# Kernel optimization log

Hardware: AMD Instinct MI355X
Metric: run time of the kernel (lower is better)

Reference implementation:

```python
import jax, jax.numpy as jnp
import numpy as np


def setup_inputs() -> dict:
    key = jax.random.key(0)
    ks = jax.random.split(key, 8)
    N, T, U = 8, 512, 64
    E, D, J, V = 512, 512, 512, 500
    s = 0.02
    return {
        "encoder_out": jax.random.normal(ks[0], (N, T, E), jnp.float32),
        "decoder_out": jax.random.normal(ks[1], (N, U, D), jnp.float32),
        "W_enc": jax.random.normal(ks[2], (J, E), jnp.float32) * s,
        "b_enc": jnp.zeros((J,), jnp.float32),
        "W_dec": jax.random.normal(ks[3], (J, D), jnp.float32) * s,
        "b_dec": jnp.zeros((J,), jnp.float32),
        "W_out": jax.random.normal(ks[4], (V, J), jnp.float32) * s,
        "b_out": jnp.zeros((V,), jnp.float32),
    }


def reference(encoder_out, decoder_out, W_enc, b_enc, W_dec, b_dec, W_out, b_out):
    # Project encoder [N,T,E]->[N,T,J] and decoder [N,U,D]->[N,U,J]
    enc = jnp.einsum("nte,je->ntj", encoder_out, W_enc) + b_enc
    dec = jnp.einsum("nud,jd->nuj", decoder_out, W_dec) + b_dec
    # Broadcast add over (T,U), tanh, then vocab projection -> [N,T,U,V]
    activations = jnp.tanh(enc[:, :, None, :] + dec[:, None, :, :])
    logits = jnp.einsum("ntuj,vj->ntuv", activations, W_out) + b_out
    return logits
```

## Files before the change

### kernel.cpp

```cpp
#include <hip/hip_runtime.h>
#include <hip/hip_bf16.h>


typedef __attribute__((ext_vector_type(4))) float f32x4;
typedef __attribute__((ext_vector_type(16))) float f32x16;
typedef __attribute__((ext_vector_type(8))) short s16x8;
typedef __attribute__((ext_vector_type(8))) unsigned short u16x8;

static __device__ __forceinline__ unsigned short f2bf(float x) {
    union { float f; unsigned u; } v; v.f = x;
    return (unsigned short)((v.u + 0x7FFFu + ((v.u >> 16) & 1u)) >> 16);
}

static __device__ __forceinline__ float bf2f(unsigned short u) {
    union { unsigned u; float f; } v; v.u = ((unsigned)u) << 16;
    return v.f;
}

static __device__ __forceinline__ float fast_tanh(float x) {
    float e = __expf(2.0f * x);
    float r = __builtin_amdgcn_rcpf(e + 1.0f);
    return __builtin_fmaf(-2.0f, r, 1.0f);
}

static __device__ __forceinline__ void lbar() {
    asm volatile("s_waitcnt lgkmcnt(0)" ::: "memory");
    __builtin_amdgcn_s_barrier();
    __builtin_amdgcn_sched_barrier(0);
}

static __device__ __forceinline__ unsigned swz64(int r, int c) {
    return (unsigned)(r * 64 + ((c ^ ((r >> 1) & 3)) << 4));
}

static __device__ void proj_body(
    const float* __restrict__ A, const float* __restrict__ W,
    const float* __restrict__ b, unsigned short* __restrict__ C,
    int mt, int jt, unsigned short* As, unsigned short* Bs)
{
    const int tid = threadIdx.x;
    const int lane = tid & 63, wid = tid >> 6;
    const int wm = wid >> 1, wn = wid & 1;

    f32x4 acc[4][4];
    const f32x4 zero = {0.f, 0.f, 0.f, 0.f};
    #pragma unroll
    for (int i = 0; i < 4; ++i)
        #pragma unroll
        for (int j = 0; j < 4; ++j) acc[i][j] = zero;

    const int c8 = (tid & 7) * 8;
    const int rbase = tid >> 3;

    for (int kt = 0; kt < 8; ++kt) {
        __syncthreads();
        #pragma unroll
        for (int p = 0; p < 4; ++p) {
            int r = p * 32 + rbase;
            int byte = (r * 128 + c8 * 2) ^ ((r & 7) << 4);
            {
                const float* s = A + (size_t)(mt * 128 + r) * 512 + kt * 64 + c8;
                f32x4 v0 = *(const f32x4*)s, v1 = *(const f32x4*)(s + 4);
                s16x8 pk;
                pk[0] = (short)f2bf(v0[0]); pk[1] = (short)f2bf(v0[1]);
                pk[2] = (short)f2bf(v0[2]); pk[3] = (short)f2bf(v0[3]);
                pk[4] = (short)f2bf(v1[0]); pk[5] = (short)f2bf(v1[1]);
                pk[6] = (short)f2bf(v1[2]); pk[7] = (short)f2bf(v1[3]);
                *(s16x8*)((char*)As + byte) = pk;
            }
            {
                const float* s = W + (size_t)(jt * 128 + r) * 512 + kt * 64 + c8;
                f32x4 v0 = *(const f32x4*)s, v1 = *(const f32x4*)(s + 4);
                s16x8 pk;
                pk[0] = (short)f2bf(v0[0]); pk[1] = (short)f2bf(v0[1]);
                pk[2] = (short)f2bf(v0[2]); pk[3] = (short)f2bf(v0[3]);
                pk[4] = (short)f2bf(v1[0]); pk[5] = (short)f2bf(v1[1]);
                pk[6] = (short)f2bf(v1[2]); pk[7] = (short)f2bf(v1[3]);
                *(s16x8*)((char*)Bs + byte) = pk;
            }
        }
        __syncthreads();
        #pragma unroll
        for (int kk = 0; kk < 2; ++kk) {
            s16x8 af[4], bfr[4];
            #pragma unroll
            for (int mi = 0; mi < 4; ++mi) {
                int row = wm * 64 + mi * 16 + (lane & 15);
                int byte = (row * 128 + kk * 64 + ((lane >> 4) * 16)) ^ ((row & 7) << 4);
                af[mi] = *(const s16x8*)((const char*)As + byte);
            }
            #pragma unroll
            for (int ni = 0; ni < 4; ++ni) {
                int row = wn * 64 + ni * 16 + (lane & 15);
                int byte = (row * 128 + kk * 64 + ((lane >> 4) * 16)) ^ ((row & 7) << 4);
                bfr[ni] = *(const s16x8*)((const char*)Bs + byte);
            }
            #pragma unroll
            for (int mi = 0; mi < 4; ++mi)
                #pragma unroll
                for (int ni = 0; ni < 4; ++ni)
                    acc[mi][ni] = __builtin_amdgcn_mfma_f32_16x16x32_bf16(
                        af[mi], bfr[ni], acc[mi][ni], 0, 0, 0);
        }
    }

    #pragma unroll
    for (int ni = 0; ni < 4; ++ni) {
        int col = jt * 128 + wn * 64 + ni * 16 + (lane & 15);
        float bias = b[col];
        #pragma unroll
        for (int mi = 0; mi < 4; ++mi) {
            int row0 = mt * 128 + wm * 64 + mi * 16 + ((lane >> 4) << 2);
            #pragma unroll
            for (int j = 0; j < 4; ++j)
                C[(size_t)(row0 + j) * 512 + col] = f2bf(acc[mi][ni][j] + bias);
        }
    }
}

__global__ __launch_bounds__(256) void prep(
    const float* __restrict__ Wout, unsigned short* __restrict__ img,
    const float* __restrict__ encoder_out, const float* __restrict__ W_enc,
    const float* __restrict__ b_enc, unsigned short* __restrict__ enc_p,
    const float* __restrict__ decoder_out, const float* __restrict__ W_dec,
    const float* __restrict__ b_dec, unsigned short* __restrict__ dec_p,
    const float* __restrict__ b_out, float* __restrict__ bpad)
{
    __shared__ unsigned short As[128 * 64];
    __shared__ unsigned short Bs[128 * 64];
    const int b = blockIdx.x;
    if (b < 128) {
        int tid = b * 256 + threadIdx.x;
        int lane = tid & 63;
        int khalf = (tid >> 6) & 1;
        int tile = (tid >> 7) & 15;
        int kt = tid >> 11;
        int v = tile * 32 + (lane & 31);
        int k = kt * 32 + khalf * 16 + (lane >> 5) * 8;
        s16x8 pk = {0, 0, 0, 0, 0, 0, 0, 0};
        if (v < 500) {
            const float* s = Wout + (size_t)v * 512 + k;
            f32x4 a = *(const f32x4*)s, c = *(const f32x4*)(s + 4);
            pk[0] = (short)f2bf(a[0]); pk[1] = (short)f2bf(a[1]);
            pk[2] = (short)f2bf(a[2]); pk[3] = (short)f2bf(a[3]);
            pk[4] = (short)f2bf(c[0]); pk[5] = (short)f2bf(c[1]);
            pk[6] = (short)f2bf(c[2]); pk[7] = (short)f2bf(c[3]);
        }
        *(s16x8*)(img + (size_t)tid * 8) = pk;
    } else if (b < 256) {
        int q = b - 128;
        proj_body(encoder_out, W_enc, b_enc, enc_p, q & 31, q >> 5, As, Bs);
    } else if (b < 272) {
        int q = b - 256;
        proj_body(decoder_out, W_dec, b_dec, dec_p, q & 3, q >> 2, As, Bs);
    } else {
        int i = threadIdx.x;
        bpad[i] = (i < 500) ? b_out[i] : 0.f;
        bpad[i + 256] = (i + 256 < 500) ? b_out[i + 256] : 0.f;
    }
}

__global__ __launch_bounds__(512, 2) void joiner_main(
    const unsigned short* __restrict__ enc, const unsigned short* __restrict__ dec,
    const unsigned short* __restrict__ Wimg, const float* __restrict__ bout,
    float* __restrict__ out)
{
    __shared__ __align__(16) char raw[66048];
    unsigned short* As0 = (unsigned short*)raw;
    unsigned short* As1 = (unsigned short*)(raw + 8192);
    float* ep = (float*)raw;

    const int bid = blockIdx.x;
    const int tid = threadIdx.x, lane = tid & 63, wn = tid >> 6;
    const int n = bid >> 8, tt = bid & 255;

    f32x16 acc[4][2];
    #pragma unroll
    for (int i = 0; i < 4; ++i)
        #pragma unroll
        for (int j = 0; j < 2; ++j)
            #pragma unroll
            for (int e = 0; e < 16; ++e) acc[i][j][e] = 0.f;

    const int r = tid >> 2;
    const int q = tid & 3;
    const int tl = r >> 6, u = r & 63;
    const unsigned short* erow = enc + ((size_t)n * 512 + tt * 2 + tl) * 512 + q * 8;
    const unsigned short* drow = dec + ((size_t)n * 64 + u) * 512 + q * 8;
    const unsigned abyte = swz64(r, q);
    const char* wbase = (const char*)Wimg + (size_t)wn * 4096 + (size_t)lane * 16;
    const int lr = lane & 31, kg = lane >> 5;

    s16x8 bc0, bc1, bc2, bc3;
    u16x8 eN, dN;
    {
        u16x8 e = *(const u16x8*)erow;
        u16x8 d = *(const u16x8*)drow;
        s16x8 p;
        #pragma unroll
        for (int i = 0; i < 8; ++i)
            p[i] = (short)f2bf(fast_tanh(bf2f(e[i]) + bf2f(d[i])));
        *(s16x8*)((char*)As0 + abyte) = p;
        eN = *(const u16x8*)(erow + 32);
        dN = *(const u16x8*)(drow + 32);
        bc0 = *(const s16x8*)(wbase);
        bc1 = *(const s16x8*)(wbase + 1024);
        bc2 = *(const s16x8*)(wbase + 2048);
        bc3 = *(const s16x8*)(wbase + 3072);
    }
    lbar();

    #pragma unroll
    for (int kt = 0; kt < 16; ++kt) {
        const char* Ac = (char*)((kt & 1) ? As1 : As0);
        char* An = (char*)((kt & 1) ? As0 : As1);

        if (kt < 15) {
            s16x8 p;
            #pragma unroll
            for (int i = 0; i < 8; ++i)
                p[i] = (short)f2bf(fast_tanh(bf2f(eN[i]) + bf2f(dN[i])));
            *(s16x8*)(An + abyte) = p;
        }
        if (kt < 14) {
            eN = *(const u16x8*)(erow + (kt + 2) * 32);
            dN = *(const u16x8*)(drow + (kt + 2) * 32);
        }
        s16x8 bn0, bn1, bn2, bn3;
        if (kt < 15) {
            const char* g = wbase + (size_t)(kt + 1) * 32768;
            bn0 = *(const s16x8*)(g);
            bn1 = *(const s16x8*)(g + 1024);
            bn2 = *(const s16x8*)(g + 2048);
            bn3 = *(const s16x8*)(g + 3072);
        }
        {
            s16x8 a0 = *(const s16x8*)(Ac + swz64(lr, kg));
            s16x8 a1 = *(const s16x8*)(Ac + swz64(32 + lr, kg));
            s16x8 a2 = *(const s16x8*)(Ac + swz64(64 + lr, kg));
            s16x8 a3 = *(const s16x8*)(Ac + swz64(96 + lr, kg));
            acc[0][0] = __builtin_amdgcn_mfma_f32_32x32x16_bf16(bc0, a0, acc[0][0], 0, 0, 0);
            acc[0][1] = __builtin_amdgcn_mfma_f32_32x32x16_bf16(bc2, a0, acc[0][1], 0, 0, 0);
            acc[1][0] = __builtin_amdgcn_mfma_f32_32x32x16_bf16(bc0, a1, acc[1][0], 0, 0, 0);
            acc[1][1] = __builtin_amdgcn_mfma_f32_32x32x16_bf16(bc2, a1, acc[1][1], 0, 0, 0);
            acc[2][0] = __builtin_amdgcn_mfma_f32_32x32x16_bf16(bc0, a2, acc[2][0], 0, 0, 0);
            acc[2][1] = __builtin_amdgcn_mfma_f32_32x32x16_bf16(bc2, a2, acc[2][1], 0, 0, 0);
            acc[3][0] = __builtin_amdgcn_mfma_f32_32x32x16_bf16(bc0, a3, acc[3][0], 0, 0, 0);
            acc[3][1] = __builtin_amdgcn_mfma_f32_32x32x16_bf16(bc2, a3, acc[3][1], 0, 0, 0);
        }
        {
            s16x8 a0 = *(const s16x8*)(Ac + swz64(lr, 2 + kg));
            s16x8 a1 = *(const s16x8*)(Ac + swz64(32 + lr, 2 + kg));
            s16x8 a2 = *(const s16x8*)(Ac + swz64(64 + lr, 2 + kg));
            s16x8 a3 = *(const s16x8*)(Ac + swz64(96 + lr, 2 + kg));
            acc[0][0] = __builtin_amdgcn_mfma_f32_32x32x16_bf16(bc1, a0, acc[0][0], 0, 0, 0);
            acc[0][1] = __builtin_amdgcn_mfma_f32_32x32x16_bf16(bc3, a0, acc[0][1], 0, 0, 0);
            acc[1][0] = __builtin_amdgcn_mfma_f32_32x32x16_bf16(bc1, a1, acc[1][0], 0, 0, 0);
            acc[1][1] = __builtin_amdgcn_mfma_f32_32x32x16_bf16(bc3, a1, acc[1][1], 0, 0, 0);
            acc[2][0] = __builtin_amdgcn_mfma_f32_32x32x16_bf16(bc1, a2, acc[2][0], 0, 0, 0);
            acc[2][1] = __builtin_amdgcn_mfma_f32_32x32x16_bf16(bc3, a2, acc[2][1], 0, 0, 0);
            acc[3][0] = __builtin_amdgcn_mfma_f32_32x32x16_bf16(bc1, a3, acc[3][0], 0, 0, 0);
            acc[3][1] = __builtin_amdgcn_mfma_f32_32x32x16_bf16(bc3, a3, acc[3][1], 0, 0, 0);
        }
        lbar();
        bc0 = bn0; bc1 = bn1; bc2 = bn2; bc3 = bn3;
    }

    const int hi4 = kg * 4;
    #pragma unroll
    for (int o = 0; o < 4; ++o) {
        if (o) lbar();
        {
            #pragma unroll
            for (int ni = 0; ni < 2; ++ni) {
                #pragma unroll
                for (int qq = 0; qq < 4; ++qq) {
                    int v4 = wn * 64 + ni * 32 + qq * 8 + hi4;
                    if (v4 < 500) {
                        f32x4 b = *(const f32x4*)(bout + v4);
                        f32x4 ov;
                        ov[0] = acc[o][ni][qq * 4 + 0] + b[0];
                        ov[1] = acc[o][ni][qq * 4 + 1] + b[1];
                        ov[2] = acc[o][ni][qq * 4 + 2] + b[2];
                        ov[3] = acc[o][ni][qq * 4 + 3] + b[3];
                        *(f32x4*)(ep + lr * 516 + v4) = ov;
                    }
                }
            }
        }
        lbar();
        const size_t base =
            (((size_t)n * 512 + tt * 2 + (o >> 1)) * 64 + (o & 1) * 32) * 500;
        #pragma unroll
        for (int i = 0; i < 8; ++i) {
            int idx = i * 512 + tid;
            if (idx < 4000) {
                int rr = idx / 125;
                int vi = (idx - rr * 125) * 4;
                f32x4 ov = *(const f32x4*)(ep + rr * 516 + vi);
                __builtin_nontemporal_store(ov, (f32x4*)(out + base + (size_t)idx * 4));
            }
        }
    }
}

extern "C" void kernel_launch(void* const* d_in, const int* in_sizes, int n_in,
                              void* d_out, int out_size, void* d_ws, size_t ws_size,
                              hipStream_t stream) {
    const float* encoder_out = (const float*)d_in[0];
    const float* decoder_out = (const float*)d_in[1];
    const float* W_enc = (const float*)d_in[2];
    const float* b_enc = (const float*)d_in[3];
    const float* W_dec = (const float*)d_in[4];
    const float* b_dec = (const float*)d_in[5];
    const float* W_out = (const float*)d_in[6];
    const float* b_out = (const float*)d_in[7];
    float* out = (float*)d_out;

    unsigned short* enc_p = (unsigned short*)d_ws;
    unsigned short* dec_p = enc_p + (size_t)4096 * 512;
    unsigned short* wimg  = dec_p + (size_t)512 * 512;
    float* bpad = (float*)(wimg + 262144);

    prep<<<dim3(273), 256, 0, stream>>>(W_out, wimg,
                                        encoder_out, W_enc, b_enc, enc_p,
                                        decoder_out, W_dec, b_dec, dec_p,
                                        b_out, bpad);
    joiner_main<<<dim3(2048), 512, 0, stream>>>(enc_p, dec_p, wimg, bpad, out);
}
```

Measured before the change: 213.9 us.

## Stagger tanh and MFMA order across waves and use packed bf16 conversion

```diff
diff --git a/kernel.cpp b/kernel.cpp
--- a/kernel.cpp
+++ b/kernel.cpp
@@ -5,6 +5,7 @@
 typedef __attribute__((ext_vector_type(4))) float f32x4;
 typedef __attribute__((ext_vector_type(16))) float f32x16;
 typedef __attribute__((ext_vector_type(8))) short s16x8;
+typedef __attribute__((ext_vector_type(4))) unsigned int u32x4;
 typedef __attribute__((ext_vector_type(8))) unsigned short u16x8;
 
 static __device__ __forceinline__ unsigned short f2bf(float x) {
@@ -23,10 +24,16 @@
     return __builtin_fmaf(-2.0f, r, 1.0f);
 }
 
+static __device__ __forceinline__ unsigned cvt_pk_bf16(float lo, float hi) {
+    unsigned r;
+    asm("v_cvt_pk_bf16_f32 %0, %1, %2" : "=v"(r) : "v"(lo), "v"(hi));
+    return r;
+}
+
 static __device__ __forceinline__ void lbar() {
     asm volatile("s_waitcnt lgkmcnt(0)" ::: "memory");
     __builtin_amdgcn_s_barrier();
-    __builtin_amdgcn_sched_barrier(0);
+    asm volatile("" ::: "memory");
 }
 
 static __device__ __forceinline__ unsigned swz64(int r, int c) {
@@ -196,11 +203,14 @@
     {
         u16x8 e = *(const u16x8*)erow;
         u16x8 d = *(const u16x8*)drow;
-        s16x8 p;
-        #pragma unroll
-        for (int i = 0; i < 8; ++i)
-            p[i] = (short)f2bf(fast_tanh(bf2f(e[i]) + bf2f(d[i])));
-        *(s16x8*)((char*)As0 + abyte) = p;
+        u32x4 p;
+        #pragma unroll
+        for (int i = 0; i < 4; ++i) {
+            float t0 = fast_tanh(bf2f(e[2 * i]) + bf2f(d[2 * i]));
+            float t1 = fast_tanh(bf2f(e[2 * i + 1]) + bf2f(d[2 * i + 1]));
+            p[i] = cvt_pk_bf16(t0, t1);
+        }
+        *(u32x4*)((char*)As0 + abyte) = p;
         eN = *(const u16x8*)(erow + 32);
         dN = *(const u16x8*)(drow + 32);
         bc0 = *(const s16x8*)(wbase);
@@ -215,17 +225,6 @@
         const char* Ac = (char*)((kt & 1) ? As1 : As0);
         char* An = (char*)((kt & 1) ? As0 : As1);
 
-        if (kt < 15) {
-            s16x8 p;
-            #pragma unroll
-            for (int i = 0; i < 8; ++i)
-                p[i] = (short)f2bf(fast_tanh(bf2f(eN[i]) + bf2f(dN[i])));
-            *(s16x8*)(An + abyte) = p;
-        }
-        if (kt < 14) {
-            eN = *(const u16x8*)(erow + (kt + 2) * 32);
-            dN = *(const u16x8*)(drow + (kt + 2) * 32);
-        }
         s16x8 bn0, bn1, bn2, bn3;
         if (kt < 15) {
             const char* g = wbase + (size_t)(kt + 1) * 32768;
@@ -234,33 +233,69 @@
             bn2 = *(const s16x8*)(g + 2048);
             bn3 = *(const s16x8*)(g + 3072);
         }
-        {
-            s16x8 a0 = *(const s16x8*)(Ac + swz64(lr, kg));
-            s16x8 a1 = *(const s16x8*)(Ac + swz64(32 + lr, kg));
-            s16x8 a2 = *(const s16x8*)(Ac + swz64(64 + lr, kg));
-            s16x8 a3 = *(const s16x8*)(Ac + swz64(96 + lr, kg));
-            acc[0][0] = __builtin_amdgcn_mfma_f32_32x32x16_bf16(bc0, a0, acc[0][0], 0, 0, 0);
-            acc[0][1] = __builtin_amdgcn_mfma_f32_32x32x16_bf16(bc2, a0, acc[0][1], 0, 0, 0);
-            acc[1][0] = __builtin_amdgcn_mfma_f32_32x32x16_bf16(bc0, a1, acc[1][0], 0, 0, 0);
-            acc[1][1] = __builtin_amdgcn_mfma_f32_32x32x16_bf16(bc2, a1, acc[1][1], 0, 0, 0);
-            acc[2][0] = __builtin_amdgcn_mfma_f32_32x32x16_bf16(bc0, a2, acc[2][0], 0, 0, 0);
-            acc[2][1] = __builtin_amdgcn_mfma_f32_32x32x16_bf16(bc2, a2, acc[2][1], 0, 0, 0);
-            acc[3][0] = __builtin_amdgcn_mfma_f32_32x32x16_bf16(bc0, a3, acc[3][0], 0, 0, 0);
-            acc[3][1] = __builtin_amdgcn_mfma_f32_32x32x16_bf16(bc2, a3, acc[3][1], 0, 0, 0);
-        }
-        {
-            s16x8 a0 = *(const s16x8*)(Ac + swz64(lr, 2 + kg));
-            s16x8 a1 = *(const s16x8*)(Ac + swz64(32 + lr, 2 + kg));
-            s16x8 a2 = *(const s16x8*)(Ac + swz64(64 + lr, 2 + kg));
-            s16x8 a3 = *(const s16x8*)(Ac + swz64(96 + lr, 2 + kg));
-            acc[0][0] = __builtin_amdgcn_mfma_f32_32x32x16_bf16(bc1, a0, acc[0][0], 0, 0, 0);
-            acc[0][1] = __builtin_amdgcn_mfma_f32_32x32x16_bf16(bc3, a0, acc[0][1], 0, 0, 0);
-            acc[1][0] = __builtin_amdgcn_mfma_f32_32x32x16_bf16(bc1, a1, acc[1][0], 0, 0, 0);
-            acc[1][1] = __builtin_amdgcn_mfma_f32_32x32x16_bf16(bc3, a1, acc[1][1], 0, 0, 0);
-            acc[2][0] = __builtin_amdgcn_mfma_f32_32x32x16_bf16(bc1, a2, acc[2][0], 0, 0, 0);
-            acc[2][1] = __builtin_amdgcn_mfma_f32_32x32x16_bf16(bc3, a2, acc[2][1], 0, 0, 0);
-            acc[3][0] = __builtin_amdgcn_mfma_f32_32x32x16_bf16(bc1, a3, acc[3][0], 0, 0, 0);
-            acc[3][1] = __builtin_amdgcn_mfma_f32_32x32x16_bf16(bc3, a3, acc[3][1], 0, 0, 0);
+
+        if ((wn & 1) == 0) {
+            #pragma unroll
+            for (int kh = 0; kh < 2; ++kh) {
+                s16x8 a0 = *(const s16x8*)(Ac + swz64(lr, kh * 2 + kg));
+                s16x8 a1 = *(const s16x8*)(Ac + swz64(32 + lr, kh * 2 + kg));
+                s16x8 a2 = *(const s16x8*)(Ac + swz64(64 + lr, kh * 2 + kg));
+                s16x8 a3 = *(const s16x8*)(Ac + swz64(96 + lr, kh * 2 + kg));
+                s16x8 b0 = kh ? bc1 : bc0, b1 = kh ? bc3 : bc2;
+                acc[0][0] = __builtin_amdgcn_mfma_f32_32x32x16_bf16(b0, a0, acc[0][0], 0, 0, 0);
+                acc[0][1] = __builtin_amdgcn_mfma_f32_32x32x16_bf16(b1, a0, acc[0][1], 0, 0, 0);
+                acc[1][0] = __builtin_amdgcn_mfma_f32_32x32x16_bf16(b0, a1, acc[1][0], 0, 0, 0);
+                acc[1][1] = __builtin_amdgcn_mfma_f32_32x32x16_bf16(b1, a1, acc[1][1], 0, 0, 0);
+                acc[2][0] = __builtin_amdgcn_mfma_f32_32x32x16_bf16(b0, a2, acc[2][0], 0, 0, 0);
+                acc[2][1] = __builtin_amdgcn_mfma_f32_32x32x16_bf16(b1, a2, acc[2][1], 0, 0, 0);
+                acc[3][0] = __builtin_amdgcn_mfma_f32_32x32x16_bf16(b0, a3, acc[3][0], 0, 0, 0);
+                acc[3][1] = __builtin_amdgcn_mfma_f32_32x32x16_bf16(b1, a3, acc[3][1], 0, 0, 0);
+            }
+            if (kt < 15) {
+                u32x4 p;
+                #pragma unroll
+                for (int i = 0; i < 4; ++i) {
+                    float t0 = fast_tanh(bf2f(eN[2 * i]) + bf2f(dN[2 * i]));
+                    float t1 = fast_tanh(bf2f(eN[2 * i + 1]) + bf2f(dN[2 * i + 1]));
+                    p[i] = cvt_pk_bf16(t0, t1);
+                }
+                *(u32x4*)(An + abyte) = p;
+            }
+            if (kt < 14) {
+                eN = *(const u16x8*)(erow + (kt + 2) * 32);
+                dN = *(const u16x8*)(drow + (kt + 2) * 32);
+            }
+        } else {
+            if (kt < 15) {
+                u32x4 p;
+                #pragma unroll
+                for (int i = 0; i < 4; ++i) {
+                    float t0 = fast_tanh(bf2f(eN[2 * i]) + bf2f(dN[2 * i]));
+                    float t1 = fast_tanh(bf2f(eN[2 * i + 1]) + bf2f(dN[2 * i + 1]));
+                    p[i] = cvt_pk_bf16(t0, t1);
+                }
+                *(u32x4*)(An + abyte) = p;
+            }
+            if (kt < 14) {
+                eN = *(const u16x8*)(erow + (kt + 2) * 32);
+                dN = *(const u16x8*)(drow + (kt + 2) * 32);
+            }
+            #pragma unroll
+            for (int kh = 0; kh < 2; ++kh) {
+                s16x8 a0 = *(const s16x8*)(Ac + swz64(lr, kh * 2 + kg));
+                s16x8 a1 = *(const s16x8*)(Ac + swz64(32 + lr, kh * 2 + kg));
+                s16x8 a2 = *(const s16x8*)(Ac + swz64(64 + lr, kh * 2 + kg));
+                s16x8 a3 = *(const s16x8*)(Ac + swz64(96 + lr, kh * 2 + kg));
+                s16x8 b0 = kh ? bc1 : bc0, b1 = kh ? bc3 : bc2;
+                acc[0][0] = __builtin_amdgcn_mfma_f32_32x32x16_bf16(b0, a0, acc[0][0], 0, 0, 0);
+                acc[0][1] = __builtin_amdgcn_mfma_f32_32x32x16_bf16(b1, a0, acc[0][1], 0, 0, 0);
+                acc[1][0] = __builtin_amdgcn_mfma_f32_32x32x16_bf16(b0, a1, acc[1][0], 0, 0, 0);
+                acc[1][1] = __builtin_amdgcn_mfma_f32_32x32x16_bf16(b1, a1, acc[1][1], 0, 0, 0);
+                acc[2][0] = __builtin_amdgcn_mfma_f32_32x32x16_bf16(b0, a2, acc[2][0], 0, 0, 0);
+                acc[2][1] = __builtin_amdgcn_mfma_f32_32x32x16_bf16(b1, a2, acc[2][1], 0, 0, 0);
+                acc[3][0] = __builtin_amdgcn_mfma_f32_32x32x16_bf16(b0, a3, acc[3][0], 0, 0, 0);
+                acc[3][1] = __builtin_amdgcn_mfma_f32_32x32x16_bf16(b1, a3, acc[3][1], 0, 0, 0);
+            }
         }
         lbar();
         bc0 = bn0; bc1 = bn1; bc2 = bn2; bc3 = bn3;
```

Measured after the change: 217.3 us. No clear change (+1.6%).
